# Optimization experiments

Hardware: AMD Instinct MI355X
Metric: run time of the kernel (lower is better)

The kernel has to match this reference:

```python
import jax, jax.numpy as jnp
import numpy as np

B, NK, DK, DQ, DV, H = 32, 2048, 512, 512, 512, 512


def setup_inputs() -> dict:
    key = jax.random.key(0)
    ks = jax.random.split(key, 6)
    s = 1.0 / np.sqrt(H)
    return {
        "Q": jax.random.normal(ks[0], (B, DQ), dtype=jnp.float32),
        "K": jax.random.normal(ks[1], (B, NK, DK), dtype=jnp.float32),
        "V": jax.random.normal(ks[2], (B, NK, DV), dtype=jnp.float32),
        "Wk": jax.random.normal(ks[3], (DK, H), dtype=jnp.float32) * s,
        "bk": jnp.zeros((H,), dtype=jnp.float32),
        "Wq": jax.random.normal(ks[4], (DQ, H), dtype=jnp.float32) * s,
        "bq": jnp.zeros((H,), dtype=jnp.float32),
        "Wh": jax.random.normal(ks[5], (H, 1), dtype=jnp.float32) * s,
        "bh": jnp.zeros((1,), dtype=jnp.float32),
    }


def reference(Q, K, V, Wk, bk, Wq, bq, Wh, bh):
    # tk: [B, NK, H]; tq: [B, 1, H] broadcasts over n_keys (dropout_p=0 -> identity)
    tk = jnp.einsum("bnk,kh->bnh", K, Wk) + bk
    tq = (Q @ Wq + bq)[:, None, :]
    # energies: [B, NK, 1] -> relu -> softmax over n_keys (dim=1)
    energies = jax.nn.relu(jnp.einsum("bnh,ho->bno", tk + tq, Wh) + bh)
    weights = jax.nn.softmax(energies, axis=1)          # [B, NK, 1]
    output = jnp.einsum("bno,bnv->bv", weights, V)      # squeezed bmm
    return output, weights[..., 0]
```

## Files before the change

### kernel.cpp

```cpp
#include <hip/hip_runtime.h>

#define NB     32
#define NKEYS  2048
#define D      512
#define NCHUNK 64
#define RPC    (NKEYS / NCHUNK)

__device__ __forceinline__ float wave_sum(float v) {
    #pragma unroll
    for (int o = 32; o > 0; o >>= 1) v += __shfl_xor(v, o);
    return v;
}

__global__ __launch_bounds__(256) void prep_kernel(const float* __restrict__ Wk,
        const float* __restrict__ Wq, const float* __restrict__ Wh,
        const float* __restrict__ Q, const float* __restrict__ bk,
        const float* __restrict__ bq, const float* __restrict__ bh,
        float* __restrict__ wkh, float* __restrict__ qacc, float* __restrict__ cbias) {
    int tid = threadIdx.x, lane = tid & 63, wv = tid >> 6;
    __shared__ float sred[8];
    if (blockIdx.x < D) {
        int dk = blockIdx.x;
        float sk = 0.f, sq = 0.f;
        #pragma unroll
        for (int h = tid; h < D; h += 256) {
            float wh = Wh[h];
            sk = fmaf(Wk[dk * D + h], wh, sk);
            sq = fmaf(Wq[dk * D + h], wh, sq);
        }
        sk = wave_sum(sk); sq = wave_sum(sq);
        if (lane == 0) { sred[wv] = sk; sred[wv + 4] = sq; }
        __syncthreads();
        if (tid == 0) wkh[dk] = sred[0] + sred[1] + sred[2] + sred[3];
        float sqt = sred[4] + sred[5] + sred[6] + sred[7];
        if (tid < NB) atomicAdd(&qacc[tid], Q[tid * D + dk] * sqt);
    } else {
        float s = 0.f;
        #pragma unroll
        for (int h = tid; h < D; h += 256) s = fmaf(bk[h] + bq[h], Wh[h], s);
        s = wave_sum(s);
        if (lane == 0) sred[wv] = s;
        __syncthreads();
        if (tid == 0) cbias[0] = sred[0] + sred[1] + sred[2] + sred[3] + bh[0];
    }
}

__global__ __launch_bounds__(256) void energy_kernel(const float* __restrict__ K,
        const float* __restrict__ wkh, const float* __restrict__ qacc,
        const float* __restrict__ cbias, float* __restrict__ p,
        float* __restrict__ outz) {
    int tid  = threadIdx.x;
    int lane = tid & 63, wv = tid >> 6;
    long row = (long)blockIdx.x * 4 + wv;
    int b = (int)(row >> 11);
    float qd = qacc[b] + cbias[0];
    const float4* kr = (const float4*)(K + row * D);
    const float4* wr = (const float4*)wkh;
    float4 k0 = kr[lane],      w0 = wr[lane];
    float4 k1 = kr[lane + 64], w1 = wr[lane + 64];
    float s = k0.x * w0.x + k0.y * w0.y + k0.z * w0.z + k0.w * w0.w
            + k1.x * w1.x + k1.y * w1.y + k1.z * w1.z + k1.w * w1.w;
    s = wave_sum(s);
    if (lane == 0) p[row] = expf(fmaxf(s + qd, 0.f));
    if (blockIdx.x < (NB * D) / 256)
        outz[blockIdx.x * 256 + tid] = 0.f;
}

__global__ __launch_bounds__(256) void weightedv_kernel(const float* __restrict__ V,
        const float* __restrict__ p, float* __restrict__ out,
        float* __restrict__ wout) {
    int chunk = blockIdx.x & (NCHUNK - 1);
    int b     = blockIdx.x >> 6;
    int tid   = threadIdx.x;
    int lane  = tid & 63, wv = tid >> 6;
    int n0    = chunk * RPC;

    const float4* pall = (const float4*)(p + b * NKEYS);
    float s = 0.f;
    #pragma unroll
    for (int i = 0; i < 2; ++i) {
        float4 v = pall[tid + i * 256];
        s += v.x + v.y + v.z + v.w;
    }
    s = wave_sum(s);
    __shared__ float sred[4];
    if (lane == 0) sred[wv] = s;
    __syncthreads();
    float inv = 1.f / (sred[0] + sred[1] + sred[2] + sred[3]);

    const float* pb = p + b * NKEYS + n0;
    float pw[RPC];
    #pragma unroll
    for (int r = 0; r < RPC; ++r) pw[r] = pb[r];
    const float2* vb = (const float2*)(V + ((long)b * NKEYS + n0) * D);
    float2 acc = {0.f, 0.f};
    #pragma unroll 8
    for (int r = 0; r < RPC; ++r) {
        float2 vv = vb[r * (D / 2) + tid];
        acc.x = fmaf(pw[r], vv.x, acc.x);
        acc.y = fmaf(pw[r], vv.y, acc.y);
    }
    acc.x *= inv; acc.y *= inv;
    atomicAdd(&out[b * D + 2 * tid],     acc.x);
    atomicAdd(&out[b * D + 2 * tid + 1], acc.y);
    if (tid < RPC) wout[b * NKEYS + n0 + tid] = pw[tid] * inv;
}

extern "C" void kernel_launch(void* const* d_in, const int* in_sizes, int n_in,
                              void* d_out, int out_size, void* d_ws, size_t ws_size,
                              hipStream_t stream) {
    const float* Q  = (const float*)d_in[0];
    const float* K  = (const float*)d_in[1];
    const float* V  = (const float*)d_in[2];
    const float* Wk = (const float*)d_in[3];
    const float* bk = (const float*)d_in[4];
    const float* Wq = (const float*)d_in[5];
    const float* bq = (const float*)d_in[6];
    const float* Wh = (const float*)d_in[7];
    const float* bh = (const float*)d_in[8];

    float* out  = (float*)d_out;
    float* wout = out + NB * D;

    float* ws    = (float*)d_ws;
    float* qacc  = ws;
    float* cbias = ws + 64;
    float* wkh   = ws + 128;
    float* pbuf  = ws + 640;

    hipMemsetAsync(ws, 0, 128 * sizeof(float), stream);
    prep_kernel<<<D + 1, 256, 0, stream>>>(Wk, Wq, Wh, Q, bk, bq, bh, wkh, qacc, cbias);
    energy_kernel<<<(NB * NKEYS) / 4, 256, 0, stream>>>(K, wkh, qacc, cbias, pbuf, out);
    weightedv_kernel<<<NB * NCHUNK, 256, 0, stream>>>(V, pbuf, out, wout);
}
```

Baseline: 63.52 us.

## Split weighted-V sum by column slices, drop atomics and memset

The weighted-V stage now gives each block one batch and a 32-column slice and loops over all 2048 keys. Partial sums are reduced in shared memory and stored directly, which removes the float atomics, the output zeroing and the workspace memset. The query projection is no longer atomically accumulated in prep; each energy block recomputes it from a precomputed Wq·Wh vector. The cost is a much smaller grid (512 blocks) and longer per-block loops with only 128-byte contiguous V reads per row, which may cut memory parallelism.

```diff
diff --git a/kernel.cpp b/kernel.cpp
--- a/kernel.cpp
+++ b/kernel.cpp
@@ -3,20 +3,24 @@
 #define NB     32
 #define NKEYS  2048
 #define D      512
-#define NCHUNK 64
-#define RPC    (NKEYS / NCHUNK)
+#define NSLICE 16
+#define SLW    (D / NSLICE)
 
 __device__ __forceinline__ float wave_sum(float v) {
     #pragma unroll
     for (int o = 32; o > 0; o >>= 1) v += __shfl_xor(v, o);
     return v;
 }
+__device__ __forceinline__ float dot8(float4 a, float4 b, float4 c, float4 d) {
+    return a.x * b.x + a.y * b.y + a.z * b.z + a.w * b.w
+         + c.x * d.x + c.y * d.y + c.z * d.z + c.w * d.w;
+}
 
 __global__ __launch_bounds__(256) void prep_kernel(const float* __restrict__ Wk,
         const float* __restrict__ Wq, const float* __restrict__ Wh,
-        const float* __restrict__ Q, const float* __restrict__ bk,
-        const float* __restrict__ bq, const float* __restrict__ bh,
-        float* __restrict__ wkh, float* __restrict__ qacc, float* __restrict__ cbias) {
+        const float* __restrict__ bk, const float* __restrict__ bq,
+        const float* __restrict__ bh,
+        float* __restrict__ wkh, float* __restrict__ wqh, float* __restrict__ cbias) {
     int tid = threadIdx.x, lane = tid & 63, wv = tid >> 6;
     __shared__ float sred[8];
     if (blockIdx.x < D) {
@@ -32,8 +36,7 @@
         if (lane == 0) { sred[wv] = sk; sred[wv + 4] = sq; }
         __syncthreads();
         if (tid == 0) wkh[dk] = sred[0] + sred[1] + sred[2] + sred[3];
-        float sqt = sred[4] + sred[5] + sred[6] + sred[7];
-        if (tid < NB) atomicAdd(&qacc[tid], Q[tid * D + dk] * sqt);
+        if (tid == 1) wqh[dk] = sred[4] + sred[5] + sred[6] + sred[7];
     } else {
         float s = 0.f;
         #pragma unroll
@@ -46,64 +49,90 @@
 }
 
 __global__ __launch_bounds__(256) void energy_kernel(const float* __restrict__ K,
-        const float* __restrict__ wkh, const float* __restrict__ qacc,
-        const float* __restrict__ cbias, float* __restrict__ p,
-        float* __restrict__ outz) {
+        const float* __restrict__ Q, const float* __restrict__ wkh,
+        const float* __restrict__ wqh, const float* __restrict__ cbias,
+        float* __restrict__ p) {
     int tid  = threadIdx.x;
     int lane = tid & 63, wv = tid >> 6;
-    long row = (long)blockIdx.x * 4 + wv;
-    int b = (int)(row >> 11);
-    float qd = qacc[b] + cbias[0];
-    const float4* kr = (const float4*)(K + row * D);
+    long row0 = (long)blockIdx.x * 4;
+    int b = (int)(row0 >> 11);
+    __shared__ float qds;
+
+    const float4* kr = (const float4*)(K + (row0 + wv) * D);
     const float4* wr = (const float4*)wkh;
-    float4 k0 = kr[lane],      w0 = wr[lane];
-    float4 k1 = kr[lane + 64], w1 = wr[lane + 64];
-    float s = k0.x * w0.x + k0.y * w0.y + k0.z * w0.z + k0.w * w0.w
-            + k1.x * w1.x + k1.y * w1.y + k1.z * w1.z + k1.w * w1.w;
+    float4 k0 = kr[lane], k1 = kr[lane + 64];
+    float4 w0 = wr[lane], w1 = wr[lane + 64];
+
+    if (wv == 0) {
+        const float4* q4  = (const float4*)(Q + b * D);
+        const float4* wq4 = (const float4*)wqh;
+        float qd = dot8(q4[lane], wq4[lane], q4[lane + 64], wq4[lane + 64]);
+        qd = wave_sum(qd);
+        if (lane == 0) qds = qd + cbias[0];
+    }
+
+    float s = dot8(k0, w0, k1, w1);
     s = wave_sum(s);
-    if (lane == 0) p[row] = expf(fmaxf(s + qd, 0.f));
-    if (blockIdx.x < (NB * D) / 256)
-        outz[blockIdx.x * 256 + tid] = 0.f;
+    __syncthreads();
+    if (lane == 0) p[row0 + wv] = expf(fmaxf(s + qds, 0.f));
 }
 
-__global__ __launch_bounds__(256) void weightedv_kernel(const float* __restrict__ V,
+__global__ __launch_bounds__(256) void vfinal_kernel(const float* __restrict__ V,
         const float* __restrict__ p, float* __restrict__ out,
         float* __restrict__ wout) {
-    int chunk = blockIdx.x & (NCHUNK - 1);
-    int b     = blockIdx.x >> 6;
-    int tid   = threadIdx.x;
-    int lane  = tid & 63, wv = tid >> 6;
-    int n0    = chunk * RPC;
+    int slice = blockIdx.x & (NSLICE - 1);
+    int b     = blockIdx.x >> 4;
+    int tid   = threadIdx.x, lane = tid & 63, wv = tid >> 6;
 
-    const float4* pall = (const float4*)(p + b * NKEYS);
+    __shared__ float pl[NKEYS];
+    __shared__ float sredf[4];
+    __shared__ float4 red[256];
+
+    const float4* p4 = (const float4*)(p + b * NKEYS);
+    float4* pl4 = (float4*)pl;
     float s = 0.f;
     #pragma unroll
     for (int i = 0; i < 2; ++i) {
-        float4 v = pall[tid + i * 256];
+        float4 v = p4[tid + i * 256];
+        pl4[tid + i * 256] = v;
         s += v.x + v.y + v.z + v.w;
     }
     s = wave_sum(s);
-    __shared__ float sred[4];
-    if (lane == 0) sred[wv] = s;
+    if (lane == 0) sredf[wv] = s;
     __syncthreads();
-    float inv = 1.f / (sred[0] + sred[1] + sred[2] + sred[3]);
+    float inv = 1.f / (sredf[0] + sredf[1] + sredf[2] + sredf[3]);
 
-    const float* pb = p + b * NKEYS + n0;
-    float pw[RPC];
-    #pragma unroll
-    for (int r = 0; r < RPC; ++r) pw[r] = pb[r];
-    const float2* vb = (const float2*)(V + ((long)b * NKEYS + n0) * D);
-    float2 acc = {0.f, 0.f};
+    int n0 = slice * (NKEYS / NSLICE);
+    if (tid < NKEYS / NSLICE) wout[b * NKEYS + n0 + tid] = pl[n0 + tid] * inv;
+
+    int v4i = tid & 7;
+    int rg  = tid >> 3;
+    const float4* vb = (const float4*)(V + (long)b * NKEYS * D);
+    int colbase = slice * (SLW / 4);
+    float4 acc = {0.f, 0.f, 0.f, 0.f};
     #pragma unroll 8
-    for (int r = 0; r < RPC; ++r) {
-        float2 vv = vb[r * (D / 2) + tid];
-        acc.x = fmaf(pw[r], vv.x, acc.x);
-        acc.y = fmaf(pw[r], vv.y, acc.y);
+    for (int pass = 0; pass < NKEYS / 32; ++pass) {
+        int n = pass * 32 + rg;
+        float w = pl[n];
+        float4 vv = vb[(long)n * (D / 4) + colbase + v4i];
+        acc.x = fmaf(w, vv.x, acc.x);
+        acc.y = fmaf(w, vv.y, acc.y);
+        acc.z = fmaf(w, vv.z, acc.z);
+        acc.w = fmaf(w, vv.w, acc.w);
     }
-    acc.x *= inv; acc.y *= inv;
-    atomicAdd(&out[b * D + 2 * tid],     acc.x);
-    atomicAdd(&out[b * D + 2 * tid + 1], acc.y);
-    if (tid < RPC) wout[b * NKEYS + n0 + tid] = pw[tid] * inv;
+
+    red[tid] = acc;
+    __syncthreads();
+    if (tid < 8) {
+        float4 a = red[tid];
+        #pragma unroll
+        for (int g = 1; g < 32; ++g) {
+            float4 c = red[g * 8 + tid];
+            a.x += c.x; a.y += c.y; a.z += c.z; a.w += c.w;
+        }
+        a.x *= inv; a.y *= inv; a.z *= inv; a.w *= inv;
+        ((float4*)(out + b * D + slice * SLW))[tid] = a;
+    }
 }
 
 extern "C" void kernel_launch(void* const* d_in, const int* in_sizes, int n_in,
@@ -123,13 +152,12 @@
     float* wout = out + NB * D;
 
     float* ws    = (float*)d_ws;
-    float* qacc  = ws;
-    float* cbias = ws + 64;
-    float* wkh   = ws + 128;
-    float* pbuf  = ws + 640;
+    float* wkh   = ws;
+    float* wqh   = ws + 512;
+    float* cbias = ws + 1024;
+    float* pbuf  = ws + 1088;
 
-    hipMemsetAsync(ws, 0, 128 * sizeof(float), stream);
-    prep_kernel<<<D + 1, 256, 0, stream>>>(Wk, Wq, Wh, Q, bk, bq, bh, wkh, qacc, cbias);
-    energy_kernel<<<(NB * NKEYS) / 4, 256, 0, stream>>>(K, wkh, qacc, cbias, pbuf, out);
-    weightedv_kernel<<<NB * NCHUNK, 256, 0, stream>>>(V, pbuf, out, wout);
+    prep_kernel<<<D + 1, 256, 0, stream>>>(Wk, Wq, Wh, bk, bq, bh, wkh, wqh, cbias);
+    energy_kernel<<<(NB * NKEYS) / 4, 256, 0, stream>>>(K, Q, wkh, wqh, cbias, pbuf);
+    vfinal_kernel<<<NB * NSLICE, 256, 0, stream>>>(V, pbuf, out, wout);
 }
```

After: 52.71 us, median of 2. -17.0%, faster.
